# Kernel optimization log

Measured on AMD Instinct MI355X. Metric: run time of the kernel, lower is better.

Reference implementation:

```python
import jax, jax.numpy as jnp
import numpy as np

HIDDEN = 4096
N_HEADS = 32
N_KV_HEADS = 8
HEAD_DIM = 128
ROPE_THETA = 10000.0


def setup_inputs() -> dict:
    key = jax.random.key(0)
    ks = jax.random.split(key, 5)
    B, S = 1, 2048
    scale = 0.02
    return {
        "hidden_states": jax.random.normal(ks[0], (B, S, HIDDEN), dtype=jnp.float32),
        "q_w": jax.random.normal(ks[1], (N_HEADS * HEAD_DIM, HIDDEN), dtype=jnp.float32) * scale,
        "k_w": jax.random.normal(ks[2], (N_KV_HEADS * HEAD_DIM, HIDDEN), dtype=jnp.float32) * scale,
        "v_w": jax.random.normal(ks[3], (N_KV_HEADS * HEAD_DIM, HIDDEN), dtype=jnp.float32) * scale,
        "o_w": jax.random.normal(ks[4], (HIDDEN, N_HEADS * HEAD_DIM), dtype=jnp.float32) * scale,
        "position_ids": jnp.arange(S, dtype=jnp.int64 if jax.config.jax_enable_x64 else jnp.int32)[None, :],
    }


def _rotate_half(x):
    h = x.shape[-1] // 2
    return jnp.concatenate((-x[..., h:], x[..., :h]), axis=-1)


def _rope_cos_sin(position_ids, dtype):
    # default rope: inv_freq = theta^(-arange(0,hd,2)/hd), attention_scaling = 1
    inv_freq = 1.0 / (ROPE_THETA ** (jnp.arange(0, HEAD_DIM, 2, dtype=jnp.float32) / HEAD_DIM))
    freqs = position_ids.astype(jnp.float32)[:, :, None] * inv_freq[None, None, :]  # [B,S,hd/2]
    emb = jnp.concatenate((freqs, freqs), axis=-1)  # [B,S,hd]
    return jnp.cos(emb).astype(dtype), jnp.sin(emb).astype(dtype)


def reference(hidden_states, q_w, k_w, v_w, o_w, position_ids):
    B, S, _ = hidden_states.shape
    n_rep = N_HEADS // N_KV_HEADS

    q = (hidden_states @ q_w.T).reshape(B, S, N_HEADS, HEAD_DIM).transpose(0, 2, 1, 3)
    k = (hidden_states @ k_w.T).reshape(B, S, N_KV_HEADS, HEAD_DIM).transpose(0, 2, 1, 3)
    v = (hidden_states @ v_w.T).reshape(B, S, N_KV_HEADS, HEAD_DIM).transpose(0, 2, 1, 3)

    cos, sin = _rope_cos_sin(position_ids, hidden_states.dtype)
    cos = cos[:, None, :, :]  # unsqueeze head dim
    sin = sin[:, None, :, :]
    q = q * cos + _rotate_half(q) * sin
    k = k * cos + _rotate_half(k) * sin

    # repeat_kv (GQA)
    k = jnp.repeat(k, n_rep, axis=1)  # [B,H,S,hd]
    v = jnp.repeat(v, n_rep, axis=1)

    scale = HEAD_DIM ** -0.5
    scores = jnp.einsum("bhqd,bhkd->bhqk", q, k) * scale  # [B,H,S,S]
    causal = jnp.tril(jnp.ones((S, S), dtype=bool))
    scores = jnp.where(causal[None, None, :, :], scores, jnp.finfo(scores.dtype).min)
    probs = jax.nn.softmax(scores, axis=-1)
    attn = jnp.einsum("bhqk,bhkd->bhqd", probs, v)  # [B,H,S,hd]

    attn = attn.transpose(0, 2, 1, 3).reshape(B, S, N_HEADS * HEAD_DIM)
    return attn @ o_w.T
```

## Files before the change

### kernel.cpp

```cpp
#include <hip/hip_runtime.h>
#include <hip/hip_bf16.h>

#define NH   32
#define NKV  8
#define HD   128
#define SL   2048
#define HID  4096
#define KVW  1024
#define QKVN 6144

typedef __attribute__((ext_vector_type(8))) short short8;
typedef __attribute__((ext_vector_type(4))) float f32x4;

static __device__ __forceinline__ unsigned short f2bf(float f){
  union { float f; unsigned int i; } v; v.f = f;
  unsigned int r = v.i + 0x7FFFu + ((v.i >> 16) & 1u);
  return (unsigned short)(r >> 16);
}
static __device__ __forceinline__ float bf2f(unsigned short u){
  union { unsigned int i; float f; } v; v.i = ((unsigned int)u) << 16; return v.f;
}
static __device__ __forceinline__ unsigned int pack2(float lo, float hi){
  return (unsigned int)f2bf(lo) | ((unsigned int)f2bf(hi) << 16);
}
static __device__ __forceinline__ unsigned int cvtpk(float lo, float hi){
  unsigned int d;
  asm("v_cvt_pk_bf16_f32 %0, %1, %2" : "=v"(d) : "v"(lo), "v"(hi));
  return d;
}

static __device__ __forceinline__ void gload_lds16(const void* g, void* l){
  __builtin_amdgcn_global_load_lds(
      (const __attribute__((address_space(1))) void*)g,
      (__attribute__((address_space(3))) void*)l,
      16, 0, 0);
}

__global__ void cast_f32_bf16(const float* __restrict__ src, uint4* __restrict__ dst, int n8){
  int stride = gridDim.x * blockDim.x;
  for (int i = blockIdx.x * blockDim.x + threadIdx.x; i < n8; i += stride){
    float4 a = ((const float4*)src)[2*i + 0];
    float4 b = ((const float4*)src)[2*i + 1];
    uint4 o;
    o.x = pack2(a.x, a.y); o.y = pack2(a.z, a.w);
    o.z = pack2(b.x, b.y); o.w = pack2(b.z, b.w);
    dst[i] = o;
  }
}

__global__ void rope_table_kernel(const int* __restrict__ pos, float2* __restrict__ tab){
  int i = blockIdx.x * blockDim.x + threadIdx.x;
  if (i >= SL * 64) return;
  int s = i >> 6, f = i & 63;
  float inv = expf(-((float)(2 * f) / 128.0f) * 9.210340371976184f);
  float ang = (float)pos[s] * inv;
  float sn, cs;
  sincosf(ang, &sn, &cs);
  tab[i] = make_float2(cs, sn);
}

__global__ void rope_apply_kernel(unsigned short* x, const float2* __restrict__ tab,
                                  int nheads, int rowstride){
  int i = blockIdx.x * blockDim.x + threadIdx.x;
  int total = SL * nheads * 8;
  if (i >= total) return;
  int fb = (i & 7) * 8;
  int t = i >> 3;
  int h = t % nheads;
  int s = t / nheads;
  size_t base = (size_t)s * rowstride + h * HD;
  short8 x1 = *(const short8*)&x[base + fb];
  short8 x2 = *(const short8*)&x[base + fb + 64];
  const float2* tb = &tab[s * 64 + fb];
  short8 o1, o2;
#pragma unroll
  for (int j = 0; j < 8; ++j){
    float2 cs = tb[j];
    float a = bf2f((unsigned short)x1[j]);
    float b = bf2f((unsigned short)x2[j]);
    o1[j] = (short)f2bf(a * cs.x - b * cs.y);
    o2[j] = (short)f2bf(b * cs.x + a * cs.y);
  }
  *(short8*)&x[base + fb]      = o1;
  *(short8*)&x[base + fb + 64] = o2;
}

template<int BN, bool F32OUT>
__global__ __launch_bounds__(256) void gemm_bt(
  const unsigned short* __restrict__ A,
  const unsigned short* __restrict__ B,
  void* __restrict__ Cp, int M, int N, int K)
{
  constexpr int NFR = BN / 32;
  __shared__ __align__(16) unsigned short As[2][128 * 32];
  __shared__ __align__(16) unsigned short Bs[2][BN * 32];
  const int tid = threadIdx.x;
  const int lane = tid & 63, wid = tid >> 6;
  const int g = lane >> 4, c15 = lane & 15;
  const int wr = wid >> 1, wc = wid & 1;

  const int gx = gridDim.x, gy = gridDim.y;
  const int nwg = gx * gy;
  const int lin = blockIdx.y * gx + blockIdx.x;
  int mb, nb;
  const int cpx = nwg >> 3;
  const int RN  = cpx >> 3;
  if (RN > 0 && (gy & 7) == 0 && (cpx & 7) == 0 && gx % RN == 0 && (8 % (gx / RN)) == 0){
    int xcd = lin & 7, j = lin >> 3;
    int nrc = gx / RN;
    int rr = xcd / nrc, rc = xcd % nrc;
    mb = rr * 8 + (j & 7);
    nb = rc * RN + (j >> 3);
  } else { mb = lin / gx; nb = lin % gx; }
  const int m0 = mb * 128, n0 = nb * BN;

  const int srowA = wid * 32 + (lane >> 2);
  const int srowB = wid * (BN / 4) + (lane >> 2);
  const int scol  = (lane & 3) * 8;
  const unsigned short* Ag = &A[(size_t)(m0 + srowA) * K + scol];
  const unsigned short* Bg = &B[(size_t)(n0 + srowB) * K + scol];
  const size_t K16 = (size_t)16 * K;

  f32x4 acc[4][NFR] = {};

  gload_lds16(Ag,       &As[0][wid * 1024]);
  gload_lds16(Ag + K16, &As[0][wid * 1024 + 512]);
#pragma unroll
  for (int q = 0; q < BN / 64; ++q)
    gload_lds16(Bg + q * K16, &Bs[0][wid * (BN / 4) * 32 + q * 512]);
  __syncthreads();

  const int nk = K >> 5;
  for (int t = 0; t < nk; ++t){
    const int cur = t & 1;
    if (t + 1 < nk){
      const unsigned short* a2 = Ag + (size_t)(t + 1) * 32;
      const unsigned short* b2 = Bg + (size_t)(t + 1) * 32;
      const int nb2 = cur ^ 1;
      gload_lds16(a2,       &As[nb2][wid * 1024]);
      gload_lds16(a2 + K16, &As[nb2][wid * 1024 + 512]);
#pragma unroll
      for (int q = 0; q < BN / 64; ++q)
        gload_lds16(b2 + q * K16, &Bs[nb2][wid * (BN / 4) * 32 + q * 512]);
    }
    short8 af[4], bfr[NFR];
#pragma unroll
    for (int m = 0; m < 4; ++m)
      af[m] = *(const short8*)(&As[cur][(wr * 64 + m * 16 + c15) * 32 + g * 8]);
#pragma unroll
    for (int n = 0; n < NFR; ++n)
      bfr[n] = *(const short8*)(&Bs[cur][(wc * (BN / 2) + n * 16 + c15) * 32 + g * 8]);
#pragma unroll
    for (int m = 0; m < 4; ++m)
#pragma unroll
      for (int n = 0; n < NFR; ++n)
        acc[m][n] = __builtin_amdgcn_mfma_f32_16x16x32_bf16(af[m], bfr[n], acc[m][n], 0, 0, 0);
    __syncthreads();
  }

#pragma unroll
  for (int m = 0; m < 4; ++m)
#pragma unroll
    for (int n = 0; n < NFR; ++n){
      int row = m0 + wr * 64 + m * 16 + g * 4;
      int col = n0 + wc * (BN / 2) + n * 16 + c15;
      f32x4 v = acc[m][n];
      if (F32OUT){
        float* C = (float*)Cp;
#pragma unroll
        for (int r = 0; r < 4; ++r) C[(size_t)(row + r) * N + col] = v[r];
      } else {
        unsigned short* C = (unsigned short*)Cp;
#pragma unroll
        for (int r = 0; r < 4; ++r) C[(size_t)(row + r) * N + col] = f2bf(v[r]);
      }
    }
}

__global__ void transpose_v_kernel(const unsigned short* __restrict__ v, int vstride,
                                   unsigned short* __restrict__ vt){
  __shared__ unsigned short t[64][65];
  int h  = blockIdx.z;
  int d0 = blockIdx.y * 64;
  int s0 = blockIdx.x * 64;
  int c  = threadIdx.x & 63;
  int r0 = threadIdx.x >> 6;
#pragma unroll
  for (int r = r0; r < 64; r += 4) t[r][c] = v[(size_t)(s0 + r) * vstride + h * HD + d0 + c];
  __syncthreads();
#pragma unroll
  for (int r = r0; r < 64; r += 4) vt[(size_t)(h * HD + d0 + r) * SL + s0 + c] = t[c][r];
}

__global__ __launch_bounds__(512, 4) void flash_attn_kernel(
  const unsigned short* __restrict__ Q,
  const unsigned short* __restrict__ Kb,
  const unsigned short* __restrict__ Vt,
  unsigned short* __restrict__ O)
{
  __shared__ __align__(16) unsigned short Ks[2][64 * 128];
  __shared__ __align__(16) unsigned short Vs[2][128 * 64];
  const int tid = threadIdx.x, lane = tid & 63, wid = tid >> 6;
  const int g = lane >> 4, c15 = lane & 15;
  const int kvh = blockIdx.x;
  const int yy = blockIdx.y;
  const int qb = (yy < 32) ? (63 - yy) : (yy - 32);
  const int h = kvh * 4 + (wid & 3);
  const int rg = wid >> 2;
  const int q0 = qb * 32;
  const int qg = q0 + rg * 16 + c15;

  short8 aq[4];
  {
    size_t qrow = (size_t)qg * QKVN + h * HD;
#pragma unroll
    for (int kk = 0; kk < 4; ++kk)
      aq[kk] = *(const short8*)(&Q[qrow + kk * 32 + g * 8]);
  }

  const int krow = tid >> 3, kcol = (tid & 7) * 8;
  const int vrow = tid >> 2, vcol = (tid & 3) * 8;
  const unsigned short* Kgb = Kb + (size_t)kvh * HD;
  const unsigned short* Vgb = Vt + ((size_t)kvh * HD + vrow) * SL;

  auto loadKV = [&](int kt, uint4& a, uint4& b, uint4& c, uint4& d){
    const unsigned short* kg = Kgb + (size_t)(kt * 64 + krow) * QKVN + kcol;
    a = *(const uint4*)kg; b = *(const uint4*)(kg + 64);
    const unsigned short* vg = Vgb + kt * 64 + vcol;
    c = *(const uint4*)vg; d = *(const uint4*)(vg + 32);
  };
  auto writeKV = [&](int buf, uint4 a, uint4 b, uint4 c, uint4 d){
    *(uint4*)((char*)&Ks[buf][0] + krow * 256 + (( kcol * 2       ) ^ ((krow & 7) << 4))) = a;
    *(uint4*)((char*)&Ks[buf][0] + krow * 256 + (((kcol * 2) + 128) ^ ((krow & 7) << 4))) = b;
    *(uint4*)((char*)&Vs[buf][0] + vrow * 128 + (( vcol * 2       ) ^ ((vrow & 7) << 4))) = c;
    *(uint4*)((char*)&Vs[buf][0] + vrow * 128 + (((vcol * 2) +  64) ^ ((vrow & 7) << 4))) = d;
  };

  float m_i = -1e30f, l_i = 0.f;
  f32x4 oacc[8];
#pragma unroll
  for (int df = 0; df < 8; ++df) oacc[df] = (f32x4){0.f, 0.f, 0.f, 0.f};

  const float scl2 = 0.08838834764831845f * 1.4426950408889634f;
  const int nt = (q0 + 31) / 64 + 1;

  uint4 kr0, kr1, vr0, vr1;
  loadKV(0, kr0, kr1, vr0, vr1);
  writeKV(0, kr0, kr1, vr0, vr1);
  if (nt > 1) loadKV(1, kr0, kr1, vr0, vr1);
  __syncthreads();

  for (int kt = 0; kt < nt; ++kt){
    const int cur = kt & 1, nxt = cur ^ 1;
    if (kt + 1 < nt) writeKV(nxt, kr0, kr1, vr0, vr1);
    if (kt + 2 < nt) loadKV(kt + 2, kr0, kr1, vr0, vr1);

    f32x4 sc[4];
    __builtin_amdgcn_s_setprio(1);
#pragma unroll
    for (int f = 0; f < 4; ++f){
      sc[f] = (f32x4){0.f, 0.f, 0.f, 0.f};
#pragma unroll
      for (int kk = 0; kk < 4; ++kk){
        short8 bk = *(const short8*)((const char*)&Ks[cur][0] + (f * 16 + c15) * 256 +
                                     ((kk * 64 + g * 16) ^ ((c15 & 7) << 4)));
        sc[f] = __builtin_amdgcn_mfma_f32_16x16x32_bf16(bk, aq[kk], sc[f], 0, 0, 0);
      }
    }
    __builtin_amdgcn_s_setprio(0);

    float p[4][4];
    if (kt * 64 + 63 <= q0 + rg * 16){
#pragma unroll
      for (int f = 0; f < 4; ++f)
#pragma unroll
        for (int r = 0; r < 4; ++r) p[f][r] = sc[f][r] * scl2;
    } else {
#pragma unroll
      for (int f = 0; f < 4; ++f)
#pragma unroll
        for (int r = 0; r < 4; ++r){
          int kvg = kt * 64 + f * 16 + g * 4 + r;
          p[f][r] = (kvg <= qg) ? sc[f][r] * scl2 : -1e30f;
        }
    }

    float pmax = p[0][0];
#pragma unroll
    for (int f = 0; f < 4; ++f)
#pragma unroll
      for (int r = 0; r < 4; ++r) pmax = fmaxf(pmax, p[f][r]);
    pmax = fmaxf(pmax, __shfl_xor(pmax, 16, 64));
    pmax = fmaxf(pmax, __shfl_xor(pmax, 32, 64));

    if (!__all(pmax - m_i <= 8.0f)){
      float mnew = fmaxf(m_i, pmax);
      float cf = exp2f(m_i - mnew);
      float cfr[4];
#pragma unroll
      for (int r = 0; r < 4; ++r) cfr[r] = __shfl(cf, (lane & 48) | (g * 4 + r), 64);
#pragma unroll
      for (int df = 0; df < 8; ++df)
#pragma unroll
        for (int r = 0; r < 4; ++r) oacc[df][r] *= cfr[r];
      l_i *= cf;
      m_i = mnew;
    }

    float lsum = 0.f;
#pragma unroll
    for (int f = 0; f < 4; ++f)
#pragma unroll
      for (int r = 0; r < 4; ++r){ float e = exp2f(p[f][r] - m_i); p[f][r] = e; lsum += e; }
    lsum += __shfl_xor(lsum, 16, 64);
    lsum += __shfl_xor(lsum, 32, 64);
    l_i += lsum;

    unsigned int pd[4][2];
#pragma unroll
    for (int f = 0; f < 4; ++f){
      pd[f][0] = cvtpk(p[f][0], p[f][1]);
      pd[f][1] = cvtpk(p[f][2], p[f][3]);
    }

    const int src0 = ((g & 1) << 5) | c15;
    const int src1 = src0 + 16;
    const bool hiF = (g >= 2);
#pragma unroll
    for (int kk = 0; kk < 2; ++kk){
      union { unsigned int u[4]; short8 s8; } pa;
#pragma unroll
      for (int pr = 0; pr < 2; ++pr){
        unsigned int a0 = __shfl((int)pd[2 * kk + 0][pr], src0, 64);
        unsigned int b0 = __shfl((int)pd[2 * kk + 1][pr], src0, 64);
        unsigned int a1 = __shfl((int)pd[2 * kk + 0][pr], src1, 64);
        unsigned int b1 = __shfl((int)pd[2 * kk + 1][pr], src1, 64);
        pa.u[pr]     = hiF ? b0 : a0;
        pa.u[2 + pr] = hiF ? b1 : a1;
      }
      __builtin_amdgcn_s_setprio(1);
#pragma unroll
      for (int df = 0; df < 8; ++df){
        short8 bv = *(const short8*)((const char*)&Vs[cur][0] + (df * 16 + c15) * 128 +
                                     ((kk * 64 + g * 16) ^ ((c15 & 7) << 4)));
        oacc[df] = __builtin_amdgcn_mfma_f32_16x16x32_bf16(pa.s8, bv, oacc[df], 0, 0, 0);
      }
      __builtin_amdgcn_s_setprio(0);
    }
    __syncthreads();
  }

  float lr[4];
#pragma unroll
  for (int r = 0; r < 4; ++r) lr[r] = __shfl(l_i, (lane & 48) | (g * 4 + r), 64);
#pragma unroll
  for (int df = 0; df < 8; ++df)
#pragma unroll
    for (int r = 0; r < 4; ++r){
      int row = q0 + rg * 16 + g * 4 + r;
      O[(size_t)row * HID + h * HD + df * 16 + c15] = f2bf(oacc[df][r] / lr[r]);
    }
}

extern "C" void kernel_launch(void* const* d_in, const int* in_sizes, int n_in,
                              void* d_out, int out_size, void* d_ws, size_t ws_size,
                              hipStream_t stream)
{
  const float* hs  = (const float*)d_in[0];
  const float* qw  = (const float*)d_in[1];
  const float* kw  = (const float*)d_in[2];
  const float* vw  = (const float*)d_in[3];
  const float* ow  = (const float*)d_in[4];
  const int*   pos = (const int*)d_in[5];

  char* w = (char*)d_ws;
  auto alloc = [&](size_t bytes){ char* p = w; w += (bytes + 255) & ~(size_t)255; return p; };
  unsigned short* xb   = (unsigned short*)alloc((size_t)SL * HID * 2);
  unsigned short* wqkv = (unsigned short*)alloc((size_t)QKVN * HID * 2);
  unsigned short* owb  = (unsigned short*)alloc((size_t)HID * HID * 2);
  unsigned short* qkv  = (unsigned short*)alloc((size_t)SL * QKVN * 2);
  unsigned short* vt   = (unsigned short*)alloc((size_t)SL * KVW * 2);
  unsigned short* ab   = (unsigned short*)alloc((size_t)SL * HID * 2);
  float2*         tab  = (float2*)alloc((size_t)SL * 64 * sizeof(float2));

  auto cast = [&](const float* s, unsigned short* d, long n){
    int n8 = (int)(n / 8);
    int blocks = (n8 + 255) / 256; if (blocks > 2048) blocks = 2048;
    cast_f32_bf16<<<blocks, 256, 0, stream>>>(s, (uint4*)d, n8);
  };
  cast(hs, xb, (long)SL * HID);
  cast(qw, wqkv,                              (long)HID * HID);
  cast(kw, wqkv + (size_t)HID * HID,          (long)KVW * HID);
  cast(vw, wqkv + (size_t)(HID + KVW) * HID,  (long)KVW * HID);
  cast(ow, owb,                               (long)HID * HID);

  rope_table_kernel<<<(SL * 64 + 255) / 256, 256, 0, stream>>>(pos, tab);

  gemm_bt<128, false><<<dim3(QKVN / 128, SL / 128), 256, 0, stream>>>(xb, wqkv, qkv, SL, QKVN, HID);

  rope_apply_kernel<<<(SL * 40 * 8 + 255) / 256, 256, 0, stream>>>(qkv, tab, 40, QKVN);

  transpose_v_kernel<<<dim3(SL / 64, HD / 64, NKV), 256, 0, stream>>>(qkv + HID + KVW, QKVN, vt);

  flash_attn_kernel<<<dim3(NKV, SL / 32), 512, 0, stream>>>(qkv, qkv + HID, vt, ab);

  gemm_bt<128, true><<<dim3(HID / 128, SL / 128), 256, 0, stream>>>(ab, owb, d_out, SL, HID, HID);
}
```

Before: 343.9 us.

## Fuse fp32 weight casting into GEMM loads and skip fully masked attention fragments

After: 357.7 us. 4.0% more time.

```diff
diff --git a/kernel.cpp b/kernel.cpp
--- a/kernel.cpp
+++ b/kernel.cpp
@@ -86,9 +86,10 @@
 }
 
 template<int BN, bool F32OUT>
-__global__ __launch_bounds__(256) void gemm_bt(
+__global__ __launch_bounds__(256) void gemm_btw(
   const unsigned short* __restrict__ A,
-  const unsigned short* __restrict__ B,
+  const float* __restrict__ B0, const float* __restrict__ B1, const float* __restrict__ B2,
+  int nsplit1, int nsplit2,
   void* __restrict__ Cp, int M, int N, int K)
 {
   constexpr int NFR = BN / 32;
@@ -114,35 +115,58 @@
   } else { mb = lin / gx; nb = lin % gx; }
   const int m0 = mb * 128, n0 = nb * BN;
 
+  const float* Bsrc; int nr0;
+  if (n0 < nsplit1)      { Bsrc = B0; nr0 = n0; }
+  else if (n0 < nsplit2) { Bsrc = B1; nr0 = n0 - nsplit1; }
+  else                   { Bsrc = B2; nr0 = n0 - nsplit2; }
+
   const int srowA = wid * 32 + (lane >> 2);
-  const int srowB = wid * (BN / 4) + (lane >> 2);
-  const int scol  = (lane & 3) * 8;
-  const unsigned short* Ag = &A[(size_t)(m0 + srowA) * K + scol];
-  const unsigned short* Bg = &B[(size_t)(n0 + srowB) * K + scol];
+  const int scolA = (lane & 3) * 8;
+  const unsigned short* Ag = &A[(size_t)(m0 + srowA) * K + scolA];
   const size_t K16 = (size_t)16 * K;
 
+  const float* Bg = Bsrc + (size_t)(nr0 + wid * (BN / 4) + (lane >> 2)) * K + (lane & 3) * 8;
+  f32x4 bq[BN / 64][2];
+  auto loadB = [&](int t){
+#pragma unroll
+    for (int q = 0; q < BN / 64; ++q){
+      const float* p = Bg + (size_t)q * 16 * K + t * 32;
+      bq[q][0] = *(const f32x4*)p;
+      bq[q][1] = *(const f32x4*)(p + 4);
+    }
+  };
+  auto writeB = [&](int buf){
+#pragma unroll
+    for (int q = 0; q < BN / 64; ++q){
+      union { unsigned int u[4]; uint4 v; } w;
+      w.u[0] = cvtpk(bq[q][0][0], bq[q][0][1]);
+      w.u[1] = cvtpk(bq[q][0][2], bq[q][0][3]);
+      w.u[2] = cvtpk(bq[q][1][0], bq[q][1][1]);
+      w.u[3] = cvtpk(bq[q][1][2], bq[q][1][3]);
+      *(uint4*)&Bs[buf][(wid * (BN / 4) + q * 16 + (lane >> 2)) * 32 + (lane & 3) * 8] = w.v;
+    }
+  };
+
   f32x4 acc[4][NFR] = {};
 
+  loadB(0);
+  writeB(0);
   gload_lds16(Ag,       &As[0][wid * 1024]);
   gload_lds16(Ag + K16, &As[0][wid * 1024 + 512]);
-#pragma unroll
-  for (int q = 0; q < BN / 64; ++q)
-    gload_lds16(Bg + q * K16, &Bs[0][wid * (BN / 4) * 32 + q * 512]);
+  loadB(1);
   __syncthreads();
 
   const int nk = K >> 5;
   for (int t = 0; t < nk; ++t){
-    const int cur = t & 1;
+    const int cur = t & 1, nxt = cur ^ 1;
     if (t + 1 < nk){
+      writeB(nxt);
       const unsigned short* a2 = Ag + (size_t)(t + 1) * 32;
-      const unsigned short* b2 = Bg + (size_t)(t + 1) * 32;
-      const int nb2 = cur ^ 1;
-      gload_lds16(a2,       &As[nb2][wid * 1024]);
-      gload_lds16(a2 + K16, &As[nb2][wid * 1024 + 512]);
-#pragma unroll
-      for (int q = 0; q < BN / 64; ++q)
-        gload_lds16(b2 + q * K16, &Bs[nb2][wid * (BN / 4) * 32 + q * 512]);
-    }
+      gload_lds16(a2,       &As[nxt][wid * 1024]);
+      gload_lds16(a2 + K16, &As[nxt][wid * 1024 + 512]);
+    }
+    if (t + 2 < nk) loadB(t + 2);
+
     short8 af[4], bfr[NFR];
 #pragma unroll
     for (int m = 0; m < 4; ++m)
@@ -209,6 +233,7 @@
   const int rg = wid >> 2;
   const int q0 = qb * 32;
   const int qg = q0 + rg * 16 + c15;
+  const int qmax = q0 + rg * 16 + 15;
 
   short8 aq[4];
   {
@@ -260,11 +285,13 @@
 #pragma unroll
     for (int f = 0; f < 4; ++f){
       sc[f] = (f32x4){0.f, 0.f, 0.f, 0.f};
-#pragma unroll
-      for (int kk = 0; kk < 4; ++kk){
-        short8 bk = *(const short8*)((const char*)&Ks[cur][0] + (f * 16 + c15) * 256 +
-                                     ((kk * 64 + g * 16) ^ ((c15 & 7) << 4)));
-        sc[f] = __builtin_amdgcn_mfma_f32_16x16x32_bf16(bk, aq[kk], sc[f], 0, 0, 0);
+      if (kt * 64 + f * 16 <= qmax){
+#pragma unroll
+        for (int kk = 0; kk < 4; ++kk){
+          short8 bk = *(const short8*)((const char*)&Ks[cur][0] + (f * 16 + c15) * 256 +
+                                       ((kk * 64 + g * 16) ^ ((c15 & 7) << 4)));
+          sc[f] = __builtin_amdgcn_mfma_f32_16x16x32_bf16(bk, aq[kk], sc[f], 0, 0, 0);
+        }
       }
     }
     __builtin_amdgcn_s_setprio(0);
@@ -328,24 +355,26 @@
     const bool hiF = (g >= 2);
 #pragma unroll
     for (int kk = 0; kk < 2; ++kk){
-      union { unsigned int u[4]; short8 s8; } pa;
-#pragma unroll
-      for (int pr = 0; pr < 2; ++pr){
-        unsigned int a0 = __shfl((int)pd[2 * kk + 0][pr], src0, 64);
-        unsigned int b0 = __shfl((int)pd[2 * kk + 1][pr], src0, 64);
-        unsigned int a1 = __shfl((int)pd[2 * kk + 0][pr], src1, 64);
-        unsigned int b1 = __shfl((int)pd[2 * kk + 1][pr], src1, 64);
-        pa.u[pr]     = hiF ? b0 : a0;
-        pa.u[2 + pr] = hiF ? b1 : a1;
+      if (kt * 64 + kk * 32 <= qmax){
+        union { unsigned int u[4]; short8 s8; } pa;
+#pragma unroll
+        for (int pr = 0; pr < 2; ++pr){
+          unsigned int a0 = __shfl((int)pd[2 * kk + 0][pr], src0, 64);
+          unsigned int b0 = __shfl((int)pd[2 * kk + 1][pr], src0, 64);
+          unsigned int a1 = __shfl((int)pd[2 * kk + 0][pr], src1, 64);
+          unsigned int b1 = __shfl((int)pd[2 * kk + 1][pr], src1, 64);
+          pa.u[pr]     = hiF ? b0 : a0;
+          pa.u[2 + pr] = hiF ? b1 : a1;
+        }
+        __builtin_amdgcn_s_setprio(1);
+#pragma unroll
+        for (int df = 0; df < 8; ++df){
+          short8 bv = *(const short8*)((const char*)&Vs[cur][0] + (df * 16 + c15) * 128 +
+                                       ((kk * 64 + g * 16) ^ ((c15 & 7) << 4)));
+          oacc[df] = __builtin_amdgcn_mfma_f32_16x16x32_bf16(pa.s8, bv, oacc[df], 0, 0, 0);
+        }
+        __builtin_amdgcn_s_setprio(0);
       }
-      __builtin_amdgcn_s_setprio(1);
-#pragma unroll
-      for (int df = 0; df < 8; ++df){
-        short8 bv = *(const short8*)((const char*)&Vs[cur][0] + (df * 16 + c15) * 128 +
-                                     ((kk * 64 + g * 16) ^ ((c15 & 7) << 4)));
-        oacc[df] = __builtin_amdgcn_mfma_f32_16x16x32_bf16(pa.s8, bv, oacc[df], 0, 0, 0);
-      }
-      __builtin_amdgcn_s_setprio(0);
     }
     __syncthreads();
   }
@@ -375,28 +404,21 @@
 
   char* w = (char*)d_ws;
   auto alloc = [&](size_t bytes){ char* p = w; w += (bytes + 255) & ~(size_t)255; return p; };
-  unsigned short* xb   = (unsigned short*)alloc((size_t)SL * HID * 2);
-  unsigned short* wqkv = (unsigned short*)alloc((size_t)QKVN * HID * 2);
-  unsigned short* owb  = (unsigned short*)alloc((size_t)HID * HID * 2);
-  unsigned short* qkv  = (unsigned short*)alloc((size_t)SL * QKVN * 2);
-  unsigned short* vt   = (unsigned short*)alloc((size_t)SL * KVW * 2);
-  unsigned short* ab   = (unsigned short*)alloc((size_t)SL * HID * 2);
-  float2*         tab  = (float2*)alloc((size_t)SL * 64 * sizeof(float2));
-
-  auto cast = [&](const float* s, unsigned short* d, long n){
-    int n8 = (int)(n / 8);
-    int blocks = (n8 + 255) / 256; if (blocks > 2048) blocks = 2048;
-    cast_f32_bf16<<<blocks, 256, 0, stream>>>(s, (uint4*)d, n8);
-  };
-  cast(hs, xb, (long)SL * HID);
-  cast(qw, wqkv,                              (long)HID * HID);
-  cast(kw, wqkv + (size_t)HID * HID,          (long)KVW * HID);
-  cast(vw, wqkv + (size_t)(HID + KVW) * HID,  (long)KVW * HID);
-  cast(ow, owb,                               (long)HID * HID);
+  unsigned short* xb  = (unsigned short*)alloc((size_t)SL * HID * 2);
+  unsigned short* qkv = (unsigned short*)alloc((size_t)SL * QKVN * 2);
+  unsigned short* vt  = (unsigned short*)alloc((size_t)SL * KVW * 2);
+  unsigned short* ab  = (unsigned short*)alloc((size_t)SL * HID * 2);
+  float2*         tab = (float2*)alloc((size_t)SL * 64 * sizeof(float2));
+
+  {
+    int n8 = SL * HID / 8;
+    cast_f32_bf16<<<2048, 256, 0, stream>>>(hs, (uint4*)xb, n8);
+  }
 
   rope_table_kernel<<<(SL * 64 + 255) / 256, 256, 0, stream>>>(pos, tab);
 
-  gemm_bt<128, false><<<dim3(QKVN / 128, SL / 128), 256, 0, stream>>>(xb, wqkv, qkv, SL, QKVN, HID);
+  gemm_btw<128, false><<<dim3(QKVN / 128, SL / 128), 256, 0, stream>>>(
+      xb, qw, kw, vw, HID, HID + KVW, qkv, SL, QKVN, HID);
 
   rope_apply_kernel<<<(SL * 40 * 8 + 255) / 256, 256, 0, stream>>>(qkv, tab, 40, QKVN);
 
@@ -404,5 +426,6 @@
 
   flash_attn_kernel<<<dim3(NKV, SL / 32), 512, 0, stream>>>(qkv, qkv + HID, vt, ab);
 
-  gemm_bt<128, true><<<dim3(HID / 128, SL / 128), 256, 0, stream>>>(ab, owb, d_out, SL, HID, HID);
-}
+  gemm_btw<128, true><<<dim3(HID / 128, SL / 128), 256, 0, stream>>>(
+      ab, ow, ow, ow, HID, HID, d_out, SL, HID, HID);
+}
```
